# Kernel tuning notes

Measured on AMD Instinct MI355X. Metric: run time of the kernel, lower is better.

The kernel has to match this reference:

```python
import jax, jax.numpy as jnp
import numpy as np

N = 100000
E = 1600000
IN_C, HID_C, OUT_C = 128, 64, 64


def setup_inputs() -> dict:
    key = jax.random.key(0)
    k1, k2, k3, k4, k5 = jax.random.split(key, 5)
    x = jax.random.normal(k1, (N, IN_C), dtype=jnp.float32)
    edge_index = jax.random.randint(k2, (2, E), 0, N, dtype=jnp.int64)
    # Glorot-style params per GCNConv (weight [in,out], bias [out])
    W1 = jax.random.normal(k3, (IN_C, HID_C), dtype=jnp.float32) / np.sqrt(IN_C)
    b1 = jnp.zeros((HID_C,), dtype=jnp.float32)
    W2 = jax.random.normal(k4, (HID_C, OUT_C), dtype=jnp.float32) / np.sqrt(HID_C)
    b2 = jnp.zeros((OUT_C,), dtype=jnp.float32)
    return {"x": x, "edge_index": edge_index, "W1": W1, "b1": b1, "W2": W2, "b2": b2}


def _gcn_norm(edge_index, n):
    # add self-loops, then symmetric normalization deg^{-1/2} A deg^{-1/2}
    loop = jnp.arange(n, dtype=edge_index.dtype)
    src = jnp.concatenate([edge_index[0], loop])
    dst = jnp.concatenate([edge_index[1], loop])
    deg = jax.ops.segment_sum(jnp.ones_like(dst, dtype=jnp.float32), dst, num_segments=n)
    dinv = jnp.where(deg > 0, jax.lax.rsqrt(deg), 0.0)
    norm = dinv[src] * dinv[dst]  # [E+N]
    return src, dst, norm


def _gcn_conv(x, W, b, src, dst, norm, n):
    h = x @ W                                   # [N, out]
    m = h[src] * norm[:, None]                  # gather + scale  [E+N, out]
    out = jax.ops.segment_sum(m, dst, num_segments=n)  # scatter-add at dst
    return out + b


def reference(x, edge_index, W1, b1, W2, b2):
    n = x.shape[0]
    src, dst, norm = _gcn_norm(edge_index, n)
    h = jax.nn.relu(_gcn_conv(x, W1, b1, src, dst, norm, n))
    out = _gcn_conv(h, W2, b2, src, dst, norm, n)
    return out
```

## Files before the change

### kernel.cpp

```cpp
#include <hip/hip_runtime.h>
#include <hip/hip_fp16.h>


#define CAP   64
#define CAPB  3072
#define BKMAX 1024

typedef _Float16 f16x8 __attribute__((ext_vector_type(8)));
typedef float f32x4 __attribute__((ext_vector_type(4)));

struct alignas(16) H8 { __half2 a, b, c, d; };

__global__ void detect_i64_kernel(const unsigned int* __restrict__ w, int ncheck,
                                  int* __restrict__ flag) {
  __shared__ int nz;
  if (threadIdx.x == 0) nz = 0;
  __syncthreads();
  for (int i = threadIdx.x; i < ncheck; i += blockDim.x) {
    if (w[2 * i + 1] != 0u) nz = 1;
  }
  __syncthreads();
  if (threadIdx.x == 0) flag[0] = (nz == 0) ? 1 : 0;
}

__global__ __launch_bounds__(256) void hist_gemm_kernel(
    const int* __restrict__ edges, int E, const int* __restrict__ flag,
    int* __restrict__ Hh, int SB, int nbk,
    int* __restrict__ tmp_pk, int* __restrict__ tmp_mt,
    const float* __restrict__ A, const float* __restrict__ W,
    __half* __restrict__ g, int n) {
  __shared__ __align__(16) char smem[34816];
  const int t = threadIdx.x;
  const int bid = (int)blockIdx.x;

  if (bid < SB) {
    int* hist = (int*)smem;
    const int f = flag[0];
    const int blk0 = bid * 2048;

    for (int i = t; i < nbk; i += 256) hist[i] = 0;
    __syncthreads();

    if (blk0 + 2048 <= E) {
      int sv[8], dv[8];
      if (f) {
#pragma unroll
        for (int u = 0; u < 4; ++u) {
          const int eg = blk0 + (u * 256 + t) * 2;
          const int4 a = *(const int4*)&edges[2 * (size_t)eg];
          const int4 b = *(const int4*)&edges[2 * ((size_t)E + eg)];
          sv[u * 2] = a.x; sv[u * 2 + 1] = a.z;
          dv[u * 2] = b.x; dv[u * 2 + 1] = b.z;
        }
      } else {
#pragma unroll
        for (int u = 0; u < 2; ++u) {
          const int eg = blk0 + (u * 256 + t) * 4;
          const int4 a = *(const int4*)&edges[eg];
          const int4 b = *(const int4*)&edges[(size_t)E + eg];
          sv[u * 4] = a.x; sv[u * 4 + 1] = a.y; sv[u * 4 + 2] = a.z; sv[u * 4 + 3] = a.w;
          dv[u * 4] = b.x; dv[u * 4 + 1] = b.y; dv[u * 4 + 2] = b.z; dv[u * 4 + 3] = b.w;
        }
      }
      int pk[8], mt[8];
#pragma unroll
      for (int i = 0; i < 8; ++i) {
        const int bk = dv[i] >> 7;
        const int rk = atomicAdd(&hist[bk], 1);
        pk[i] = ((dv[i] & 127) << 17) | sv[i];
        mt[i] = bk | (rk << 10);
      }
      if (f) {
#pragma unroll
        for (int u = 0; u < 4; ++u) {
          const int eg = blk0 + (u * 256 + t) * 2;
          *(int2*)&tmp_pk[eg] = make_int2(pk[u * 2], pk[u * 2 + 1]);
          *(int2*)&tmp_mt[eg] = make_int2(mt[u * 2], mt[u * 2 + 1]);
        }
      } else {
        *(int4*)&tmp_pk[blk0 + t * 4]        = make_int4(pk[0], pk[1], pk[2], pk[3]);
        *(int4*)&tmp_pk[blk0 + 1024 + t * 4] = make_int4(pk[4], pk[5], pk[6], pk[7]);
        *(int4*)&tmp_mt[blk0 + t * 4]        = make_int4(mt[0], mt[1], mt[2], mt[3]);
        *(int4*)&tmp_mt[blk0 + 1024 + t * 4] = make_int4(mt[4], mt[5], mt[6], mt[7]);
      }
    } else {
      for (int e = blk0 + t; e < E; e += 256) {
        const int s = f ? edges[2 * (size_t)e] : edges[e];
        const int d = f ? edges[2 * ((size_t)E + e)] : edges[(size_t)E + e];
        const int bk = d >> 7;
        const int rk = atomicAdd(&hist[bk], 1);
        tmp_pk[e] = ((d & 127) << 17) | s;
        tmp_mt[e] = bk | (rk << 10);
      }
    }
    __syncthreads();
    for (int i = t; i < nbk; i += 256) Hh[(size_t)i * SB + bid] = hist[i];
    return;
  }

  _Float16 (*Af)[136] = (_Float16(*)[136])smem;
  _Float16 (*Wf)[136] = (_Float16(*)[136])(smem + 17408);
  const int row0 = (bid - SB) * 64;

  {
    const int r = t >> 2, k0 = (t & 3) << 5;
    const int gr = row0 + r;
    if (gr < n) {
#pragma unroll
      for (int q = 0; q < 4; ++q) {
        float4 a = *(const float4*)&A[(size_t)gr * 128 + k0 + q * 8];
        float4 b = *(const float4*)&A[(size_t)gr * 128 + k0 + q * 8 + 4];
        f16x8 v;
        v[0] = (_Float16)a.x; v[1] = (_Float16)a.y; v[2] = (_Float16)a.z; v[3] = (_Float16)a.w;
        v[4] = (_Float16)b.x; v[5] = (_Float16)b.y; v[6] = (_Float16)b.z; v[7] = (_Float16)b.w;
        *(f16x8*)&Af[r][k0 + q * 8] = v;
      }
    } else {
      f16x8 z = {0, 0, 0, 0, 0, 0, 0, 0};
#pragma unroll
      for (int q = 0; q < 4; ++q) *(f16x8*)&Af[r][k0 + q * 8] = z;
    }
  }
  {
    const int c = t & 63, kq = t >> 6;
#pragma unroll
    for (int i = 0; i < 32; ++i)
      Wf[c][kq * 32 + i] = (_Float16)W[(size_t)(kq * 32 + i) * 64 + c];
  }
  __syncthreads();

  const int wid = t >> 6, lane = t & 63;
  const int lr = lane & 15, kg = lane >> 4;
  f32x4 acc[4] = {{0, 0, 0, 0}, {0, 0, 0, 0}, {0, 0, 0, 0}, {0, 0, 0, 0}};
#pragma unroll
  for (int kc = 0; kc < 4; ++kc) {
    f16x8 av = *(const f16x8*)&Af[wid * 16 + lr][kc * 32 + kg * 8];
#pragma unroll
    for (int ct = 0; ct < 4; ++ct) {
      f16x8 bv = *(const f16x8*)&Wf[ct * 16 + lr][kc * 32 + kg * 8];
      acc[ct] = __builtin_amdgcn_mfma_f32_16x16x32_f16(av, bv, acc[ct], 0, 0, 0);
    }
  }
#pragma unroll
  for (int ct = 0; ct < 4; ++ct) {
#pragma unroll
    for (int rg = 0; rg < 4; ++rg) {
      const int r = row0 + wid * 16 + kg * 4 + rg;
      if (r < n) g[(size_t)r * 64 + ct * 16 + lr] = (__half)(float)acc[ct][rg];
    }
  }
}

__global__ __launch_bounds__(256) void scan_hist_kernel(
    int* __restrict__ Hh, int SB, int* __restrict__ T) {
  __shared__ int sm[256];
  __shared__ int carry;
  const int b = blockIdx.x;
  const int t = threadIdx.x;
  if (t == 0) carry = 0;
  __syncthreads();
  int* __restrict__ row = Hh + (size_t)b * SB;
  for (int base = 0; base < SB; base += 256) {
    const int i = base + t;
    const int v = (i < SB) ? row[i] : 0;
    sm[t] = v;
    __syncthreads();
    for (int off = 1; off < 256; off <<= 1) {
      int u = (t >= off) ? sm[t - off] : 0;
      __syncthreads();
      sm[t] += u;
      __syncthreads();
    }
    const int excl = sm[t] - v + carry;
    if (i < SB) row[i] = excl;
    __syncthreads();
    if (t == 0) carry += sm[255];
    __syncthreads();
  }
  if (t == 0) T[b] = carry;
}

__global__ __launch_bounds__(256) void place_kernel(
    const int* __restrict__ tmp_pk, const int* __restrict__ tmp_mt,
    const int* __restrict__ Hh, int SB, int E, int* __restrict__ arena) {
  const int e0 = ((int)blockIdx.x * 256 + (int)threadIdx.x) * 4;
  if (e0 >= E) return;
  const int blk = e0 >> 11;
  if (e0 + 4 <= E) {
    const int4 pk = *(const int4*)&tmp_pk[e0];
    const int4 mt = *(const int4*)&tmp_mt[e0];
    const int b0 = mt.x & 1023, b1 = mt.y & 1023, b2 = mt.z & 1023, b3 = mt.w & 1023;
    const int p0 = Hh[(size_t)b0 * SB + blk] + (mt.x >> 10);
    const int p1 = Hh[(size_t)b1 * SB + blk] + (mt.y >> 10);
    const int p2 = Hh[(size_t)b2 * SB + blk] + (mt.z >> 10);
    const int p3 = Hh[(size_t)b3 * SB + blk] + (mt.w >> 10);
    if (p0 < CAPB) arena[(size_t)b0 * CAPB + p0] = pk.x;
    if (p1 < CAPB) arena[(size_t)b1 * CAPB + p1] = pk.y;
    if (p2 < CAPB) arena[(size_t)b2 * CAPB + p2] = pk.z;
    if (p3 < CAPB) arena[(size_t)b3 * CAPB + p3] = pk.w;
  } else {
    for (int e = e0; e < E; ++e) {
      const int mt = tmp_mt[e];
      const int bk = mt & 1023;
      const int p = Hh[(size_t)bk * SB + blk] + (mt >> 10);
      if (p < CAPB) arena[(size_t)bk * CAPB + p] = tmp_pk[e];
    }
  }
}

__global__ __launch_bounds__(512) void cluster_csr_kernel(
    const int* __restrict__ T, const int* __restrict__ arena,
    int n, int* __restrict__ counts, float* __restrict__ dinv,
    int* __restrict__ csrp) {
  __shared__ int lc[128];
  const int b = blockIdx.x;
  const int t = threadIdx.x;
  if (t < 128) lc[t] = 0;
  __syncthreads();
  int cnt = T[b];
  if (cnt > CAPB) cnt = CAPB;
  const int* __restrict__ seg = &arena[(size_t)b * CAPB];
  for (int j = t; j < cnt; j += 512) {
    const int p = seg[j];
    const int dl = p >> 17;
    const int s = p & 131071;
    const int r = atomicAdd(&lc[dl], 1);
    if (r < CAP) csrp[((size_t)(b << 7) + dl) * CAP + r] = s;
  }
  __syncthreads();
  const int d = (b << 7) + t;
  if (t < 128 && d < n) {
    counts[d] = lc[t];
    dinv[d] = rsqrtf((float)(lc[t] + 1));
  }
}

__global__ __launch_bounds__(256) void agg1_kernel(
    const __half* __restrict__ hs, const int* __restrict__ counts,
    const int* __restrict__ csrp, const float* __restrict__ dinv,
    const float* __restrict__ bias, __half* __restrict__ out, int n) {
  const int wid = blockIdx.x * 4 + ((int)threadIdx.x >> 6);
  if (wid * 8 >= n) return;
  const int lane = (int)threadIdx.x & 63;
  const int og = lane >> 3;
  const int gl = lane & 7;
  const int d = wid * 8 + og;
  const bool active = d < n;
  const int dc = active ? d : n - 1;

  int len = counts[dc];
  if (len > CAP) len = CAP;
  if (!active) len = 0;
  const int* __restrict__ row = &csrp[(size_t)dc * CAP];
  const float dd = dinv[dc];

  H8 sv = *(const H8*)&hs[(size_t)dc * 64 + (gl << 3)];
  float acc[8];
  {
    float2 f0 = __half22float2(sv.a), f1 = __half22float2(sv.b);
    float2 f2 = __half22float2(sv.c), f3 = __half22float2(sv.d);
    acc[0] = dd * f0.x; acc[1] = dd * f0.y; acc[2] = dd * f1.x; acc[3] = dd * f1.y;
    acc[4] = dd * f2.x; acc[5] = dd * f2.y; acc[6] = dd * f3.x; acc[7] = dd * f3.y;
  }

  for (int j = 0; __any(j < len); j += 8) {
    int sidx[8];
    bool pr[8];
#pragma unroll
    for (int u = 0; u < 8; ++u) {
      pr[u] = (j + u) < len;
      sidx[u] = pr[u] ? row[j + u] : dc;
    }
    H8 v[8];
#pragma unroll
    for (int u = 0; u < 8; ++u) v[u] = *(const H8*)&hs[(size_t)sidx[u] * 64 + (gl << 3)];
#pragma unroll
    for (int u = 0; u < 8; ++u) {
      const float w = pr[u] ? dinv[sidx[u]] : 0.f;
      float2 g0 = __half22float2(v[u].a), g1 = __half22float2(v[u].b);
      float2 g2 = __half22float2(v[u].c), g3 = __half22float2(v[u].d);
      acc[0] = fmaf(w, g0.x, acc[0]); acc[1] = fmaf(w, g0.y, acc[1]);
      acc[2] = fmaf(w, g1.x, acc[2]); acc[3] = fmaf(w, g1.y, acc[3]);
      acc[4] = fmaf(w, g2.x, acc[4]); acc[5] = fmaf(w, g2.y, acc[5]);
      acc[6] = fmaf(w, g3.x, acc[6]); acc[7] = fmaf(w, g3.y, acc[7]);
    }
  }

  if (active) {
    const float4 b0 = *(const float4*)&bias[gl << 3];
    const float4 b1 = *(const float4*)&bias[(gl << 3) + 4];
    float o[8];
    o[0] = fmaf(acc[0], dd, b0.x); o[1] = fmaf(acc[1], dd, b0.y);
    o[2] = fmaf(acc[2], dd, b0.z); o[3] = fmaf(acc[3], dd, b0.w);
    o[4] = fmaf(acc[4], dd, b1.x); o[5] = fmaf(acc[5], dd, b1.y);
    o[6] = fmaf(acc[6], dd, b1.z); o[7] = fmaf(acc[7], dd, b1.w);
#pragma unroll
    for (int c = 0; c < 8; ++c) o[c] = fmaxf(o[c], 0.f);
    H8 hv;
    hv.a = __floats2half2_rn(o[0], o[1]); hv.b = __floats2half2_rn(o[2], o[3]);
    hv.c = __floats2half2_rn(o[4], o[5]); hv.d = __floats2half2_rn(o[6], o[7]);
    *(H8*)&out[(size_t)d * 64 + (gl << 3)] = hv;
  }
}

__global__ __launch_bounds__(256) void agg2_gemm_kernel(
    const __half* __restrict__ hh, const int* __restrict__ counts,
    const int* __restrict__ csrp, const float* __restrict__ dinv,
    const float* __restrict__ W2, const float* __restrict__ b2,
    float* __restrict__ out, int n) {
  __shared__ __align__(16) _Float16 Wf[64][88];
  __shared__ __align__(16) _Float16 Ac[32][88];
  const int t = threadIdx.x;

  {
    const int c = t & 63, kq = t >> 6;
#pragma unroll
    for (int i = 0; i < 16; ++i)
      Wf[c][kq * 16 + i] = (_Float16)W2[(size_t)(kq * 16 + i) * 64 + c];
  }

  const int wid = t >> 6;
  const int lane = t & 63;
  const int og = lane >> 3, gl = lane & 7;
  const int node0 = (int)blockIdx.x * 32;
  const int d = node0 + wid * 8 + og;
  const bool active = d < n;
  const int dc = active ? d : n - 1;

  int len = counts[dc];
  if (len > CAP) len = CAP;
  if (!active) len = 0;
  const int* __restrict__ row = &csrp[(size_t)dc * CAP];
  const float dd = dinv[dc];

  H8 sv = *(const H8*)&hh[(size_t)dc * 64 + (gl << 3)];
  float acc[8];
  {
    float2 f0 = __half22float2(sv.a), f1 = __half22float2(sv.b);
    float2 f2 = __half22float2(sv.c), f3 = __half22float2(sv.d);
    acc[0] = dd * f0.x; acc[1] = dd * f0.y; acc[2] = dd * f1.x; acc[3] = dd * f1.y;
    acc[4] = dd * f2.x; acc[5] = dd * f2.y; acc[6] = dd * f3.x; acc[7] = dd * f3.y;
  }

  for (int j = 0; __any(j < len); j += 8) {
    int sidx[8];
    bool pr[8];
#pragma unroll
    for (int u = 0; u < 8; ++u) {
      pr[u] = (j + u) < len;
      sidx[u] = pr[u] ? row[j + u] : dc;
    }
    H8 v[8];
#pragma unroll
    for (int u = 0; u < 8; ++u) v[u] = *(const H8*)&hh[(size_t)sidx[u] * 64 + (gl << 3)];
#pragma unroll
    for (int u = 0; u < 8; ++u) {
      const float w = pr[u] ? dinv[sidx[u]] : 0.f;
      float2 g0 = __half22float2(v[u].a), g1 = __half22float2(v[u].b);
      float2 g2 = __half22float2(v[u].c), g3 = __half22float2(v[u].d);
      acc[0] = fmaf(w, g0.x, acc[0]); acc[1] = fmaf(w, g0.y, acc[1]);
      acc[2] = fmaf(w, g1.x, acc[2]); acc[3] = fmaf(w, g1.y, acc[3]);
      acc[4] = fmaf(w, g2.x, acc[4]); acc[5] = fmaf(w, g2.y, acc[5]);
      acc[6] = fmaf(w, g3.x, acc[6]); acc[7] = fmaf(w, g3.y, acc[7]);
    }
  }

  {
    const int lrow = wid * 8 + og;
    f16x8 av;
#pragma unroll
    for (int c = 0; c < 8; ++c) av[c] = (_Float16)(acc[c] * dd);
    *(f16x8*)&Ac[lrow][gl << 3] = av;
  }
  __syncthreads();

  const int lr = lane & 15, kg = lane >> 4;
  const int rt = wid >> 1;
  const int ct0 = (wid & 1) * 2;
#pragma unroll
  for (int cti = 0; cti < 2; ++cti) {
    const int ct = ct0 + cti;
    f32x4 c4 = {0, 0, 0, 0};
#pragma unroll
    for (int kc = 0; kc < 2; ++kc) {
      f16x8 a = *(const f16x8*)&Ac[rt * 16 + lr][kc * 32 + kg * 8];
      f16x8 b = *(const f16x8*)&Wf[ct * 16 + lr][kc * 32 + kg * 8];
      c4 = __builtin_amdgcn_mfma_f32_16x16x32_f16(a, b, c4, 0, 0, 0);
    }
    const float bb = b2[ct * 16 + lr];
#pragma unroll
    for (int rg = 0; rg < 4; ++rg) {
      const int r = node0 + rt * 16 + kg * 4 + rg;
      if (r < n) out[(size_t)r * 64 + ct * 16 + lr] = (float)c4[rg] + bb;
    }
  }
}

extern "C" void kernel_launch(void* const* d_in, const int* in_sizes, int n_in,
                              void* d_out, int out_size, void* d_ws, size_t ws_size,
                              hipStream_t stream) {
  const float* x  = (const float*)d_in[0];
  const int*   ei = (const int*)d_in[1];
  const float* W1 = (const float*)d_in[2];
  const float* b1 = (const float*)d_in[3];
  const float* W2 = (const float*)d_in[4];
  const float* b2 = (const float*)d_in[5];
  float* out = (float*)d_out;

  const int N = in_sizes[0] / 128;
  const int E = in_sizes[1] / 2;
  const int NBK = (N + 127) >> 7;
  const int SB = (E + 2047) / 2048;
  const int G1 = (N + 63) / 64;

  char* ws = (char*)d_ws;
  size_t off = 0;
  auto take = [&](size_t bytes) -> void* {
    void* p = ws + off;
    off += (bytes + 255) & ~(size_t)255;
    return p;
  };
  int*    flag   = (int*)take(sizeof(int));
  int*    Hh     = (int*)take((size_t)NBK * SB * 4);
  int*    T      = (int*)take((size_t)NBK * 4);
  int*    counts = (int*)take((size_t)N * 4);
  float*  dinv   = (float*)take((size_t)N * 4);
  int*    tmp_pk = (int*)take((size_t)E * 4);
  int*    tmp_mt = (int*)take((size_t)E * 4);
  int*    arena  = (int*)take((size_t)NBK * CAPB * 4);
  int*    csrp   = (int*)take((size_t)N * CAP * 4);
  __half* hsf    = (__half*)take((size_t)N * 64 * 2);
  __half* hh     = (__half*)take((size_t)N * 64 * 2);
  (void)ws_size; (void)n_in; (void)out_size;

  detect_i64_kernel<<<1, 256, 0, stream>>>((const unsigned int*)ei, 4096, flag);

  hist_gemm_kernel<<<SB + G1, 256, 0, stream>>>(
      ei, E, flag, Hh, SB, NBK, tmp_pk, tmp_mt, x, W1, hsf, N);

  scan_hist_kernel<<<NBK, 256, 0, stream>>>(Hh, SB, T);

  place_kernel<<<((E + 3) / 4 + 255) / 256, 256, 0, stream>>>(
      tmp_pk, tmp_mt, Hh, SB, E, arena);

  cluster_csr_kernel<<<NBK, 512, 0, stream>>>(T, arena, N, counts, dinv, csrp);

  agg1_kernel<<<(N + 31) / 32, 256, 0, stream>>>(
      hsf, counts, csrp, dinv, b1, hh, N);

  agg2_gemm_kernel<<<(N + 31) / 32, 256, 0, stream>>>(
      hh, counts, csrp, dinv, W2, b2, out, N);
}
```

Measured before the change: 147.6 us.

## Build per-bucket CSR in shared memory inside aggregation kernels, drop global CSR

Replaces the cluster kernel that wrote a padded global CSR (N×64 ints) with a small degree/dinv kernel. Each aggregation kernel now rebuilds its 128-node bucket's adjacency lists in LDS from the arena, then gathers. This removes the global CSR write and its re-reads in both layers, in exchange for doing the bucket clustering twice. Blocks grow to 512 threads covering 128 nodes, with about 33KB+ of LDS, which may lower occupancy. Neighbor order within each row is now nondeterministic per pass, but the results are the same up to float summation order.

```diff
diff --git a/kernel.cpp b/kernel.cpp
--- a/kernel.cpp
+++ b/kernel.cpp
@@ -208,13 +208,33 @@
   }
 }
 
-__global__ __launch_bounds__(512) void cluster_csr_kernel(
+__global__ __launch_bounds__(256) void count_dinv_kernel(
     const int* __restrict__ T, const int* __restrict__ arena,
-    int n, int* __restrict__ counts, float* __restrict__ dinv,
-    int* __restrict__ csrp) {
+    int n, float* __restrict__ dinv) {
   __shared__ int lc[128];
   const int b = blockIdx.x;
   const int t = threadIdx.x;
+  if (t < 128) lc[t] = 0;
+  __syncthreads();
+  int cnt = T[b];
+  if (cnt > CAPB) cnt = CAPB;
+  const int* __restrict__ seg = &arena[(size_t)b * CAPB];
+  for (int j = t; j < cnt; j += 256) atomicAdd(&lc[seg[j] >> 17], 1);
+  __syncthreads();
+  const int d = (b << 7) + t;
+  if (t < 128 && d < n) dinv[d] = rsqrtf((float)(lc[t] + 1));
+}
+
+__global__ __launch_bounds__(512) void agg1_fused_kernel(
+    const __half* __restrict__ hs, const int* __restrict__ T,
+    const int* __restrict__ arena, const float* __restrict__ dinv,
+    const float* __restrict__ bias, __half* __restrict__ out, int n) {
+  __shared__ int lc[128];
+  __shared__ int rows[128][65];
+  const int b = blockIdx.x;
+  const int t = threadIdx.x;
+  const int node0 = b << 7;
+
   if (t < 128) lc[t] = 0;
   __syncthreads();
   int cnt = T[b];
@@ -223,169 +243,178 @@
   for (int j = t; j < cnt; j += 512) {
     const int p = seg[j];
     const int dl = p >> 17;
-    const int s = p & 131071;
     const int r = atomicAdd(&lc[dl], 1);
-    if (r < CAP) csrp[((size_t)(b << 7) + dl) * CAP + r] = s;
-  }
-  __syncthreads();
-  const int d = (b << 7) + t;
-  if (t < 128 && d < n) {
-    counts[d] = lc[t];
-    dinv[d] = rsqrtf((float)(lc[t] + 1));
-  }
-}
-
-__global__ __launch_bounds__(256) void agg1_kernel(
-    const __half* __restrict__ hs, const int* __restrict__ counts,
-    const int* __restrict__ csrp, const float* __restrict__ dinv,
-    const float* __restrict__ bias, __half* __restrict__ out, int n) {
-  const int wid = blockIdx.x * 4 + ((int)threadIdx.x >> 6);
-  if (wid * 8 >= n) return;
-  const int lane = (int)threadIdx.x & 63;
-  const int og = lane >> 3;
-  const int gl = lane & 7;
-  const int d = wid * 8 + og;
-  const bool active = d < n;
-  const int dc = active ? d : n - 1;
-
-  int len = counts[dc];
-  if (len > CAP) len = CAP;
-  if (!active) len = 0;
-  const int* __restrict__ row = &csrp[(size_t)dc * CAP];
-  const float dd = dinv[dc];
-
-  H8 sv = *(const H8*)&hs[(size_t)dc * 64 + (gl << 3)];
-  float acc[8];
-  {
-    float2 f0 = __half22float2(sv.a), f1 = __half22float2(sv.b);
-    float2 f2 = __half22float2(sv.c), f3 = __half22float2(sv.d);
-    acc[0] = dd * f0.x; acc[1] = dd * f0.y; acc[2] = dd * f1.x; acc[3] = dd * f1.y;
-    acc[4] = dd * f2.x; acc[5] = dd * f2.y; acc[6] = dd * f3.x; acc[7] = dd * f3.y;
-  }
-
-  for (int j = 0; __any(j < len); j += 8) {
-    int sidx[8];
-    bool pr[8];
-#pragma unroll
-    for (int u = 0; u < 8; ++u) {
-      pr[u] = (j + u) < len;
-      sidx[u] = pr[u] ? row[j + u] : dc;
-    }
-    H8 v[8];
-#pragma unroll
-    for (int u = 0; u < 8; ++u) v[u] = *(const H8*)&hs[(size_t)sidx[u] * 64 + (gl << 3)];
-#pragma unroll
-    for (int u = 0; u < 8; ++u) {
-      const float w = pr[u] ? dinv[sidx[u]] : 0.f;
-      float2 g0 = __half22float2(v[u].a), g1 = __half22float2(v[u].b);
-      float2 g2 = __half22float2(v[u].c), g3 = __half22float2(v[u].d);
-      acc[0] = fmaf(w, g0.x, acc[0]); acc[1] = fmaf(w, g0.y, acc[1]);
-      acc[2] = fmaf(w, g1.x, acc[2]); acc[3] = fmaf(w, g1.y, acc[3]);
-      acc[4] = fmaf(w, g2.x, acc[4]); acc[5] = fmaf(w, g2.y, acc[5]);
-      acc[6] = fmaf(w, g3.x, acc[6]); acc[7] = fmaf(w, g3.y, acc[7]);
-    }
-  }
-
-  if (active) {
-    const float4 b0 = *(const float4*)&bias[gl << 3];
-    const float4 b1 = *(const float4*)&bias[(gl << 3) + 4];
-    float o[8];
-    o[0] = fmaf(acc[0], dd, b0.x); o[1] = fmaf(acc[1], dd, b0.y);
-    o[2] = fmaf(acc[2], dd, b0.z); o[3] = fmaf(acc[3], dd, b0.w);
-    o[4] = fmaf(acc[4], dd, b1.x); o[5] = fmaf(acc[5], dd, b1.y);
-    o[6] = fmaf(acc[6], dd, b1.z); o[7] = fmaf(acc[7], dd, b1.w);
-#pragma unroll
-    for (int c = 0; c < 8; ++c) o[c] = fmaxf(o[c], 0.f);
-    H8 hv;
-    hv.a = __floats2half2_rn(o[0], o[1]); hv.b = __floats2half2_rn(o[2], o[3]);
-    hv.c = __floats2half2_rn(o[4], o[5]); hv.d = __floats2half2_rn(o[6], o[7]);
-    *(H8*)&out[(size_t)d * 64 + (gl << 3)] = hv;
-  }
-}
-
-__global__ __launch_bounds__(256) void agg2_gemm_kernel(
-    const __half* __restrict__ hh, const int* __restrict__ counts,
-    const int* __restrict__ csrp, const float* __restrict__ dinv,
+    if (r < CAP) rows[dl][r] = p & 131071;
+  }
+  __syncthreads();
+
+  const int wave = t >> 6;
+  const int og = (t & 63) >> 3;
+  const int gl = t & 7;
+
+#pragma unroll
+  for (int pass = 0; pass < 2; ++pass) {
+    const int local = pass * 64 + wave * 8 + og;
+    const int d = node0 + local;
+    const bool active = d < n;
+    const int dcl = active ? local : 0;
+    const int dc = node0 + dcl;
+    int len = lc[dcl];
+    if (len > CAP) len = CAP;
+    if (!active) len = 0;
+    const float dd = dinv[dc];
+
+    H8 sv = *(const H8*)&hs[(size_t)dc * 64 + (gl << 3)];
+    float acc[8];
+    {
+      float2 f0 = __half22float2(sv.a), f1 = __half22float2(sv.b);
+      float2 f2 = __half22float2(sv.c), f3 = __half22float2(sv.d);
+      acc[0] = dd * f0.x; acc[1] = dd * f0.y; acc[2] = dd * f1.x; acc[3] = dd * f1.y;
+      acc[4] = dd * f2.x; acc[5] = dd * f2.y; acc[6] = dd * f3.x; acc[7] = dd * f3.y;
+    }
+
+    for (int j = 0; __any(j < len); j += 8) {
+      int sidx[8];
+      bool pr[8];
+#pragma unroll
+      for (int u = 0; u < 8; ++u) {
+        pr[u] = (j + u) < len;
+        sidx[u] = pr[u] ? rows[dcl][j + u] : dc;
+      }
+      H8 v[8];
+#pragma unroll
+      for (int u = 0; u < 8; ++u) v[u] = *(const H8*)&hs[(size_t)sidx[u] * 64 + (gl << 3)];
+#pragma unroll
+      for (int u = 0; u < 8; ++u) {
+        const float w = pr[u] ? dinv[sidx[u]] : 0.f;
+        float2 g0 = __half22float2(v[u].a), g1 = __half22float2(v[u].b);
+        float2 g2 = __half22float2(v[u].c), g3 = __half22float2(v[u].d);
+        acc[0] = fmaf(w, g0.x, acc[0]); acc[1] = fmaf(w, g0.y, acc[1]);
+        acc[2] = fmaf(w, g1.x, acc[2]); acc[3] = fmaf(w, g1.y, acc[3]);
+        acc[4] = fmaf(w, g2.x, acc[4]); acc[5] = fmaf(w, g2.y, acc[5]);
+        acc[6] = fmaf(w, g3.x, acc[6]); acc[7] = fmaf(w, g3.y, acc[7]);
+      }
+    }
+
+    if (active) {
+      const float4 b0 = *(const float4*)&bias[gl << 3];
+      const float4 b1 = *(const float4*)&bias[(gl << 3) + 4];
+      float o[8];
+      o[0] = fmaf(acc[0], dd, b0.x); o[1] = fmaf(acc[1], dd, b0.y);
+      o[2] = fmaf(acc[2], dd, b0.z); o[3] = fmaf(acc[3], dd, b0.w);
+      o[4] = fmaf(acc[4], dd, b1.x); o[5] = fmaf(acc[5], dd, b1.y);
+      o[6] = fmaf(acc[6], dd, b1.z); o[7] = fmaf(acc[7], dd, b1.w);
+#pragma unroll
+      for (int c = 0; c < 8; ++c) o[c] = fmaxf(o[c], 0.f);
+      H8 hv;
+      hv.a = __floats2half2_rn(o[0], o[1]); hv.b = __floats2half2_rn(o[2], o[3]);
+      hv.c = __floats2half2_rn(o[4], o[5]); hv.d = __floats2half2_rn(o[6], o[7]);
+      *(H8*)&out[(size_t)d * 64 + (gl << 3)] = hv;
+    }
+  }
+}
+
+__global__ __launch_bounds__(512) void agg2_fused_kernel(
+    const __half* __restrict__ hh, const int* __restrict__ T,
+    const int* __restrict__ arena, const float* __restrict__ dinv,
     const float* __restrict__ W2, const float* __restrict__ b2,
     float* __restrict__ out, int n) {
-  __shared__ __align__(16) _Float16 Wf[64][88];
-  __shared__ __align__(16) _Float16 Ac[32][88];
+  __shared__ int lc[128];
+  __shared__ int rows[128][65];
+  __shared__ __align__(16) _Float16 Wf[64][72];
+  __shared__ __align__(16) _Float16 Ac[128][72];
+  const int b = blockIdx.x;
   const int t = threadIdx.x;
-
+  const int node0 = b << 7;
+
+  if (t < 128) lc[t] = 0;
   {
     const int c = t & 63, kq = t >> 6;
 #pragma unroll
-    for (int i = 0; i < 16; ++i)
-      Wf[c][kq * 16 + i] = (_Float16)W2[(size_t)(kq * 16 + i) * 64 + c];
-  }
-
-  const int wid = t >> 6;
+    for (int i = 0; i < 8; ++i)
+      Wf[c][kq * 8 + i] = (_Float16)W2[(size_t)(kq * 8 + i) * 64 + c];
+  }
+  __syncthreads();
+  int cnt = T[b];
+  if (cnt > CAPB) cnt = CAPB;
+  const int* __restrict__ seg = &arena[(size_t)b * CAPB];
+  for (int j = t; j < cnt; j += 512) {
+    const int p = seg[j];
+    const int dl = p >> 17;
+    const int r = atomicAdd(&lc[dl], 1);
+    if (r < CAP) rows[dl][r] = p & 131071;
+  }
+  __syncthreads();
+
+  const int wave = t >> 6;
+  const int og = (t & 63) >> 3;
+  const int gl = t & 7;
+
+#pragma unroll
+  for (int pass = 0; pass < 2; ++pass) {
+    const int local = pass * 64 + wave * 8 + og;
+    const int d = node0 + local;
+    const bool active = d < n;
+    const int dcl = active ? local : 0;
+    const int dc = node0 + dcl;
+    int len = lc[dcl];
+    if (len > CAP) len = CAP;
+    if (!active) len = 0;
+    const float dd = dinv[dc];
+
+    H8 sv = *(const H8*)&hh[(size_t)dc * 64 + (gl << 3)];
+    float acc[8];
+    {
+      float2 f0 = __half22float2(sv.a), f1 = __half22float2(sv.b);
+      float2 f2 = __half22float2(sv.c), f3 = __half22float2(sv.d);
+      acc[0] = dd * f0.x; acc[1] = dd * f0.y; acc[2] = dd * f1.x; acc[3] = dd * f1.y;
+      acc[4] = dd * f2.x; acc[5] = dd * f2.y; acc[6] = dd * f3.x; acc[7] = dd * f3.y;
+    }
+
+    for (int j = 0; __any(j < len); j += 8) {
+      int sidx[8];
+      bool pr[8];
+#pragma unroll
+      for (int u = 0; u < 8; ++u) {
+        pr[u] = (j + u) < len;
+        sidx[u] = pr[u] ? rows[dcl][j + u] : dc;
+      }
+      H8 v[8];
+#pragma unroll
+      for (int u = 0; u < 8; ++u) v[u] = *(const H8*)&hh[(size_t)sidx[u] * 64 + (gl << 3)];
+#pragma unroll
+      for (int u = 0; u < 8; ++u) {
+        const float w = pr[u] ? dinv[sidx[u]] : 0.f;
+        float2 g0 = __half22float2(v[u].a), g1 = __half22float2(v[u].b);
+        float2 g2 = __half22float2(v[u].c), g3 = __half22float2(v[u].d);
+        acc[0] = fmaf(w, g0.x, acc[0]); acc[1] = fmaf(w, g0.y, acc[1]);
+        acc[2] = fmaf(w, g1.x, acc[2]); acc[3] = fmaf(w, g1.y, acc[3]);
+        acc[4] = fmaf(w, g2.x, acc[4]); acc[5] = fmaf(w, g2.y, acc[5]);
+        acc[6] = fmaf(w, g3.x, acc[6]); acc[7] = fmaf(w, g3.y, acc[7]);
+      }
+    }
+
+    {
+      f16x8 av;
+#pragma unroll
+      for (int c = 0; c < 8; ++c) av[c] = active ? (_Float16)(acc[c] * dd) : (_Float16)0.f;
+      *(f16x8*)&Ac[local][gl << 3] = av;
+    }
+  }
+  __syncthreads();
+
   const int lane = t & 63;
-  const int og = lane >> 3, gl = lane & 7;
-  const int node0 = (int)blockIdx.x * 32;
-  const int d = node0 + wid * 8 + og;
-  const bool active = d < n;
-  const int dc = active ? d : n - 1;
-
-  int len = counts[dc];
-  if (len > CAP) len = CAP;
-  if (!active) len = 0;
-  const int* __restrict__ row = &csrp[(size_t)dc * CAP];
-  const float dd = dinv[dc];
-
-  H8 sv = *(const H8*)&hh[(size_t)dc * 64 + (gl << 3)];
-  float acc[8];
-  {
-    float2 f0 = __half22float2(sv.a), f1 = __half22float2(sv.b);
-    float2 f2 = __half22float2(sv.c), f3 = __half22float2(sv.d);
-    acc[0] = dd * f0.x; acc[1] = dd * f0.y; acc[2] = dd * f1.x; acc[3] = dd * f1.y;
-    acc[4] = dd * f2.x; acc[5] = dd * f2.y; acc[6] = dd * f3.x; acc[7] = dd * f3.y;
-  }
-
-  for (int j = 0; __any(j < len); j += 8) {
-    int sidx[8];
-    bool pr[8];
-#pragma unroll
-    for (int u = 0; u < 8; ++u) {
-      pr[u] = (j + u) < len;
-      sidx[u] = pr[u] ? row[j + u] : dc;
-    }
-    H8 v[8];
-#pragma unroll
-    for (int u = 0; u < 8; ++u) v[u] = *(const H8*)&hh[(size_t)sidx[u] * 64 + (gl << 3)];
-#pragma unroll
-    for (int u = 0; u < 8; ++u) {
-      const float w = pr[u] ? dinv[sidx[u]] : 0.f;
-      float2 g0 = __half22float2(v[u].a), g1 = __half22float2(v[u].b);
-      float2 g2 = __half22float2(v[u].c), g3 = __half22float2(v[u].d);
-      acc[0] = fmaf(w, g0.x, acc[0]); acc[1] = fmaf(w, g0.y, acc[1]);
-      acc[2] = fmaf(w, g1.x, acc[2]); acc[3] = fmaf(w, g1.y, acc[3]);
-      acc[4] = fmaf(w, g2.x, acc[4]); acc[5] = fmaf(w, g2.y, acc[5]);
-      acc[6] = fmaf(w, g3.x, acc[6]); acc[7] = fmaf(w, g3.y, acc[7]);
-    }
-  }
-
-  {
-    const int lrow = wid * 8 + og;
-    f16x8 av;
-#pragma unroll
-    for (int c = 0; c < 8; ++c) av[c] = (_Float16)(acc[c] * dd);
-    *(f16x8*)&Ac[lrow][gl << 3] = av;
-  }
-  __syncthreads();
-
   const int lr = lane & 15, kg = lane >> 4;
-  const int rt = wid >> 1;
-  const int ct0 = (wid & 1) * 2;
-#pragma unroll
-  for (int cti = 0; cti < 2; ++cti) {
-    const int ct = ct0 + cti;
+#pragma unroll
+  for (int i = 0; i < 4; ++i) {
+    const int idx = wave * 4 + i;
+    const int rt = idx >> 2, ct = idx & 3;
     f32x4 c4 = {0, 0, 0, 0};
 #pragma unroll
     for (int kc = 0; kc < 2; ++kc) {
       f16x8 a = *(const f16x8*)&Ac[rt * 16 + lr][kc * 32 + kg * 8];
-      f16x8 b = *(const f16x8*)&Wf[ct * 16 + lr][kc * 32 + kg * 8];
-      c4 = __builtin_amdgcn_mfma_f32_16x16x32_f16(a, b, c4, 0, 0, 0);
+      f16x8 bf = *(const f16x8*)&Wf[ct * 16 + lr][kc * 32 + kg * 8];
+      c4 = __builtin_amdgcn_mfma_f32_16x16x32_f16(a, bf, c4, 0, 0, 0);
     }
     const float bb = b2[ct * 16 + lr];
 #pragma unroll
@@ -423,12 +452,10 @@
   int*    flag   = (int*)take(sizeof(int));
   int*    Hh     = (int*)take((size_t)NBK * SB * 4);
   int*    T      = (int*)take((size_t)NBK * 4);
-  int*    counts = (int*)take((size_t)N * 4);
   float*  dinv   = (float*)take((size_t)N * 4);
   int*    tmp_pk = (int*)take((size_t)E * 4);
   int*    tmp_mt = (int*)take((size_t)E * 4);
   int*    arena  = (int*)take((size_t)NBK * CAPB * 4);
-  int*    csrp   = (int*)take((size_t)N * CAP * 4);
   __half* hsf    = (__half*)take((size_t)N * 64 * 2);
   __half* hh     = (__half*)take((size_t)N * 64 * 2);
   (void)ws_size; (void)n_in; (void)out_size;
@@ -443,11 +470,9 @@
   place_kernel<<<((E + 3) / 4 + 255) / 256, 256, 0, stream>>>(
       tmp_pk, tmp_mt, Hh, SB, E, arena);
 
-  cluster_csr_kernel<<<NBK, 512, 0, stream>>>(T, arena, N, counts, dinv, csrp);
-
-  agg1_kernel<<<(N + 31) / 32, 256, 0, stream>>>(
-      hsf, counts, csrp, dinv, b1, hh, N);
-
-  agg2_gemm_kernel<<<(N + 31) / 32, 256, 0, stream>>>(
-      hh, counts, csrp, dinv, W2, b2, out, N);
-}
+  count_dinv_kernel<<<NBK, 256, 0, stream>>>(T, arena, N, dinv);
+
+  agg1_fused_kernel<<<NBK, 512, 0, stream>>>(hsf, T, arena, dinv, b1, hh, N);
+
+  agg2_fused_kernel<<<NBK, 512, 0, stream>>>(hh, T, arena, dinv, W2, b2, out, N);
+}
```

New measurement: 149.2 us. About the same (+1.1%).
